# Performance work log

Measured on AMD Instinct MI355X. Metric: run time of the kernel, lower is better.

Reference implementation:

```python
import jax, jax.numpy as jnp
import numpy as np

B, S, H, E, ID, OD, RD = 128, 256, 512, 128, 30000, 64, 32
IN = H + E + 1 + OD  # rnn_input_dim: weighted + embedded + rate + online feats


def setup_inputs() -> dict:
    key = jax.random.key(0)
    ks = jax.random.split(key, 18)
    sc = 0.02
    inp = {}
    inp['input_id'] = jax.random.randint(ks[0], (B, 1), 0, ID, dtype=jnp.int32)
    inp['input_rate'] = jax.random.uniform(ks[1], (B, 1), jnp.float32)
    inp['hidden'] = jax.random.normal(ks[2], (1, B, H), jnp.float32) * 0.1
    inp['encoder_outputs'] = jax.random.normal(ks[3], (S, B, H), jnp.float32) * 0.1
    inp['attn_mask'] = (jax.random.uniform(ks[4], (B, S)) > 0.3).astype(jnp.int32).at[:, 0].set(1)
    inp['constraint_vec'] = (jax.random.uniform(ks[5], (B, ID)) > 0.5).astype(jnp.float32).at[:, 0].set(1.0)
    inp['online_features'] = jax.random.normal(ks[6], (B, OD), jnp.float32) * 0.1
    inp['rid_features'] = jax.random.normal(ks[7], (B, RD), jnp.float32) * 0.1
    inp['emb'] = jax.random.normal(ks[8], (ID, E), jnp.float32) * sc
    inp['attn_W'] = jax.random.normal(ks[9], (2 * H, H), jnp.float32) * sc
    inp['attn_b'] = jnp.zeros((H,), jnp.float32)
    inp['v_W'] = jax.random.normal(ks[10], (H,), jnp.float32) * sc
    inp['W_ih'] = jax.random.normal(ks[11], (3 * H, IN), jnp.float32) * sc
    inp['b_ih'] = jnp.zeros((3 * H,), jnp.float32)
    inp['W_hh'] = jax.random.normal(ks[12], (3 * H, H), jnp.float32) * sc
    inp['b_hh'] = jnp.zeros((3 * H,), jnp.float32)
    inp['fc_id_W'] = jax.random.normal(ks[13], (ID, H), jnp.float32) * sc
    inp['fc_id_b'] = jnp.zeros((ID,), jnp.float32)
    inp['tan_W'] = jax.random.normal(ks[14], (H, E + H), jnp.float32) * sc
    inp['tan_b'] = jnp.zeros((H,), jnp.float32)
    inp['rate_W'] = jax.random.normal(ks[15], (1, H + RD), jnp.float32) * sc
    inp['rate_b'] = jnp.zeros((1,), jnp.float32)
    return inp


def reference(input_id, input_rate, hidden, encoder_outputs, attn_mask, constraint_vec,
              online_features, rid_features, emb, attn_W, attn_b, v_W, W_ih, b_ih,
              W_hh, b_hh, fc_id_W, fc_id_b, tan_W, tan_b, rate_W, rate_b):
    h = hidden[0]                                    # [B,H]
    embedded = emb[input_id[:, 0]]                   # [B,E] (dropout p=0 -> identity)
    # --- attention ---
    enc = jnp.transpose(encoder_outputs, (1, 0, 2))  # [B,S,H]
    hid_rep = jnp.broadcast_to(h[:, None, :], (B, S, H))
    energy = jnp.tanh(jnp.concatenate([hid_rep, enc], axis=2) @ attn_W + attn_b)  # [B,S,H]
    score = energy @ v_W                             # [B,S]
    score = jnp.where(attn_mask == 0, jnp.float32(-1e10), score)
    a = jax.nn.softmax(score, axis=1)                # [B,S]
    weighted = jnp.einsum('bs,bsh->bh', a, enc)      # [B,H]
    # --- GRU step (torch gate order r,z,n) ---
    rnn_in = jnp.concatenate([weighted, embedded, input_rate, online_features], axis=1)  # [B,IN]
    gi = rnn_in @ W_ih.T + b_ih                      # [B,3H]
    gh = h @ W_hh.T + b_hh                           # [B,3H]
    r = jax.nn.sigmoid(gi[:, :H] + gh[:, :H])
    z = jax.nn.sigmoid(gi[:, H:2 * H] + gh[:, H:2 * H])
    n = jnp.tanh(gi[:, 2 * H:] + r * gh[:, 2 * H:])
    h_new = (1.0 - z) * n + z * h                    # [B,H]
    # --- masked log softmax over id_size ---
    logits = h_new @ fc_id_W.T + fc_id_b             # [B,ID]
    maxes = jnp.max(logits, axis=1, keepdims=True)
    x_exp = jnp.exp(logits - maxes) * constraint_vec
    x_sum = jnp.sum(x_exp, axis=1, keepdims=True)
    ratio_safe = jnp.where(constraint_vec > 0, x_exp / x_sum, 1.0)
    prediction_id = jnp.where(constraint_vec > 0, jnp.log(ratio_safe), -jnp.inf)  # [B,ID]
    # --- tandem rate head ---
    max_id = jnp.argmax(prediction_id, axis=1)
    id_emb = emb[max_id]                             # [B,E]
    rate_in = jax.nn.relu(jnp.concatenate([id_emb, h_new], axis=1) @ tan_W.T + tan_b)  # [B,H]
    prediction_rate = jax.nn.sigmoid(jnp.concatenate([rate_in, rid_features], axis=1) @ rate_W.T + rate_b)  # [B,1]
    return prediction_id, prediction_rate, h_new[None]  # hidden: [1,B,H]
```

## Files before the change

### kernel.cpp

```cpp
#include <hip/hip_runtime.h>
#include <math.h>

typedef __attribute__((ext_vector_type(8))) short short8;
typedef __attribute__((ext_vector_type(4))) float f32x4;
typedef __attribute__((ext_vector_type(4))) unsigned int u32x4;

constexpr int kB  = 128;
constexpr int kS  = 256;
constexpr int kH  = 512;
constexpr int kE  = 128;
constexpr int kID = 30000;
constexpr int kOD = 64;
constexpr int kRD = 32;
constexpr int kIN = kH + kE + 1 + kOD;
constexpr int kG  = 3 * kH;
constexpr int kNC = 10;

constexpr int O_PRE  = 0;
constexpr int O_RNN  = O_PRE + kB * kH;
constexpr int O_GI   = O_RNN + kB * kIN;
constexpr int O_GH   = O_GI + kB * kG;
constexpr int O_HNEW = O_GH + kB * kG;
constexpr int O_W2F  = O_HNEW + kB * kH;
constexpr int O_AH   = O_W2F + 32 * 4096;
constexpr int O_AL   = O_AH + 8 * 4096;
constexpr int O_SM   = O_AL + 8 * 4096;
constexpr int O_SS   = O_SM + kB * kNC;
constexpr int O_SBV  = O_SS + kB * kNC;
constexpr int O_SBI  = O_SBV + kB * kNC;
constexpr int O_ENCF = O_SBI + kB * kNC;
constexpr int O_SC8  = O_GI;
constexpr int O_GP   = O_ENCF;
constexpr int O_GPH  = O_GP + 8 * kB * kG;
constexpr int O_RP   = O_PRE;

constexpr float kNegSentinel = -1.0e30f;

__device__ __forceinline__ float fast_tanh(float x) {
    float e = __expf(2.f * x);
    return 1.f - 2.f / (e + 1.f);
}
__device__ __forceinline__ unsigned int f2bf(float x) {
    unsigned int u = __builtin_bit_cast(unsigned int, x);
    return (u + 0x7fffu + ((u >> 16) & 1u)) >> 16;
}
__device__ __forceinline__ float bfval(float x) {
    return __builtin_bit_cast(float, f2bf(x) << 16);
}
__device__ __forceinline__ unsigned int pack2(float a, float b) {
    return f2bf(a) | (f2bf(b) << 16);
}

__global__ __launch_bounds__(256) void k_prep(
    const float* __restrict__ enc, const float* __restrict__ attn_W,
    const float* __restrict__ attn_b, const float* __restrict__ hidden,
    float* __restrict__ ws, unsigned int* __restrict__ wsu) {
    __shared__ unsigned int SMEM[16 * 260];
    const int blk = blockIdx.x;
    const int tid = threadIdx.x;
    if (blk < 256) {
        const int l16 = tid & 15;
        const int cb0 = ((tid >> 4) & 3) * 8 + (tid >> 6) * 32;
        const float* base = enc + ((size_t)(blk * 8) * 16 + l16) * kH + cb0;
        unsigned int* dstb = wsu + O_ENCF + (size_t)(blk * 8) * 4096;
        float4 a[2][8];
        auto ld = [&](int buf, int t) {
            const float* rp = base + (size_t)t * 16 * kH;
#pragma unroll
            for (int p = 0; p < 4; ++p) {
                a[buf][2 * p]     = *(const float4*)(rp + p * 128);
                a[buf][2 * p + 1] = *(const float4*)(rp + p * 128 + 4);
            }
        };
        auto stt = [&](int buf, int t) {
            unsigned int* d = dstb + (size_t)t * 4096;
#pragma unroll
            for (int p = 0; p < 4; ++p) {
                float4 x = a[buf][2 * p], y = a[buf][2 * p + 1];
                u32x4 o = {pack2(x.x, x.y), pack2(x.z, x.w),
                           pack2(y.x, y.y), pack2(y.z, y.w)};
                *(u32x4*)(d + (p * 256 + tid) * 4) = o;
            }
        };
        ld(0, 0);
#pragma unroll
        for (int t = 0; t < 8; ++t) {
            if (t < 7) ld((t + 1) & 1, t + 1);
            stt(t & 1, t);
        }
    } else if (blk < 288) {
        const int rbh = blk - 256;
        const int h0 = rbh * 16;
        const int hh = tid & 15, pg = tid >> 4;
#pragma unroll
        for (int pass = 0; pass < 16; ++pass) {
            int p = pg + pass * 16;
            float a = attn_W[(kH + 2 * p) * kH + h0 + hh];
            float b = attn_W[(kH + 2 * p + 1) * kH + h0 + hh];
            SMEM[hh * 260 + p] = pack2(a, b);
        }
        __syncthreads();
        unsigned int* dst = wsu + O_W2F + (size_t)rbh * 4096;
#pragma unroll
        for (int pass = 0; pass < 4; ++pass) {
            int idx4 = pass * 256 + tid;
            int l16 = idx4 & 15, quad = (idx4 >> 4) & 3, step = idx4 >> 6;
            const unsigned int* p = &SMEM[l16 * 260 + step * 16 + quad * 4];
            u32x4 v = {p[0], p[1], p[2], p[3]};
            *(u32x4*)(dst + idx4 * 4) = v;
        }
    } else {
        float* hl = (float*)SMEM;
        int idx = blk - 288;
        int b = idx >> 1, half = idx & 1;
        int h = half * 256 + tid;
        hl[tid]       = hidden[b * kH + tid];
        hl[tid + 256] = hidden[b * kH + tid + 256];
        __syncthreads();
        float acc0 = attn_b[h], acc1 = 0.f;
        for (int k0 = 0; k0 < kH; k0 += 16) {
            float wv[16];
#pragma unroll
            for (int j = 0; j < 16; ++j) wv[j] = attn_W[(k0 + j) * kH + h];
#pragma unroll
            for (int j = 0; j < 8; ++j) {
                acc0 += hl[k0 + j] * wv[j];
                acc1 += hl[k0 + 8 + j] * wv[8 + j];
            }
        }
        ws[O_PRE + b * kH + h] = acc0 + acc1;
    }
}

__global__ __launch_bounds__(256) void k_attn(
    const unsigned int* __restrict__ encf, const unsigned int* __restrict__ w2f,
    const float* __restrict__ vW, float* __restrict__ ws) {
    __shared__ float red[128 * 33];
    const int i = blockIdx.x;
    const int s    = (i & 7) + 8 * (i >> 6);
    const int hblk = (i >> 3) & 7;
    const int tid = threadIdx.x;
    const int w = tid >> 6, L = tid & 63;
    const int quad = L >> 4, l16 = L & 15;
    const int wm = w >> 1, wn = w & 1;
    const unsigned int* ap[4];
    const unsigned int* bp[2];
#pragma unroll
    for (int mt = 0; mt < 4; ++mt)
        ap[mt] = encf + (size_t)(s * 8 + wm * 4 + mt) * 4096 + L * 4;
#pragma unroll
    for (int nt = 0; nt < 2; ++nt)
        bp[nt] = w2f + (size_t)(hblk * 4 + wn * 2 + nt) * 4096 + L * 4;
    f32x4 acc[4][2] = {};
    u32x4 abuf[2][4], bbuf[2][2];
#pragma unroll
    for (int t = 0; t < 4; ++t) abuf[0][t] = *(const u32x4*)(ap[t]);
#pragma unroll
    for (int t = 0; t < 2; ++t) bbuf[0][t] = *(const u32x4*)(bp[t]);
#pragma unroll
    for (int step = 0; step < 16; ++step) {
        const int cur = step & 1, nxt = cur ^ 1;
        if (step < 15) {
            const int off = (step + 1) * 256;
#pragma unroll
            for (int t = 0; t < 4; ++t) abuf[nxt][t] = *(const u32x4*)(ap[t] + off);
#pragma unroll
            for (int t = 0; t < 2; ++t) bbuf[nxt][t] = *(const u32x4*)(bp[t] + off);
        }
#pragma unroll
        for (int mt = 0; mt < 4; ++mt)
#pragma unroll
            for (int nt = 0; nt < 2; ++nt)
                acc[mt][nt] = __builtin_amdgcn_mfma_f32_16x16x32_bf16(
                    __builtin_bit_cast(short8, abuf[cur][mt]),
                    __builtin_bit_cast(short8, bbuf[cur][nt]), acc[mt][nt], 0, 0, 0);
    }
#pragma unroll
    for (int mt = 0; mt < 4; ++mt)
#pragma unroll
        for (int rg = 0; rg < 4; ++rg) {
            int row = wm * 64 + mt * 16 + quad * 4 + rg;
            const float* prep = &ws[O_PRE + row * kH + hblk * 64 + wn * 32];
            const float* vp = &vW[hblk * 64 + wn * 32];
            float p = 0.f;
#pragma unroll
            for (int nt = 0; nt < 2; ++nt) {
                int hc = nt * 16 + l16;
                p += vp[hc] * fast_tanh(acc[mt][nt][rg] + prep[hc]);
            }
            red[row * 33 + wn * 16 + l16] = p;
        }
    __syncthreads();
    if (tid < 128) {
        float sum = 0.f;
#pragma unroll
        for (int c = 0; c < 32; ++c) sum += red[tid * 33 + c];
        ws[O_SC8 + hblk * (kB * kS) + tid * kS + s] = sum;
    }
}

__global__ __launch_bounds__(256) void k_soft_weight(
    const float* __restrict__ enc, const int* __restrict__ mask,
    const int* __restrict__ input_id, const float* __restrict__ input_rate,
    const float* __restrict__ online, const float* __restrict__ emb,
    float* __restrict__ ws) {
    int b = blockIdx.x, hg = blockIdx.y, tid = threadIdx.x;
    __shared__ float aa[kS];
    __shared__ float sm[256];
    __shared__ float4 red4[16 * 16];
    float v = 0.f;
#pragma unroll
    for (int h8 = 0; h8 < 8; ++h8)
        v += ws[O_SC8 + h8 * (kB * kS) + b * kS + tid];
    if (mask[b * kS + tid] == 0) v = -1e10f;
    sm[tid] = v;
    __syncthreads();
    for (int o = 128; o > 0; o >>= 1) {
        if (tid < o) sm[tid] = fmaxf(sm[tid], sm[tid + o]);
        __syncthreads();
    }
    float M = sm[0];
    __syncthreads();
    float e = __expf(v - M);
    sm[tid] = e;
    __syncthreads();
    for (int o = 128; o > 0; o >>= 1) {
        if (tid < o) sm[tid] += sm[tid + o];
        __syncthreads();
    }
    aa[tid] = e / sm[0];
    __syncthreads();
    int lane = tid & 15, sg = tid >> 4;
    int col4 = hg * 16 + lane;
    const float4* enc4 = (const float4*)enc;
    float4 acc = {0.f, 0.f, 0.f, 0.f};
    for (int s = sg; s < kS; s += 16) {
        float a = aa[s];
        float4 e4 = enc4[(s * kB + b) * (kH / 4) + col4];
        acc.x += a * e4.x; acc.y += a * e4.y; acc.z += a * e4.z; acc.w += a * e4.w;
    }
    red4[sg * 16 + lane] = acc;
    __syncthreads();
    if (sg == 0) {
        float4 o = {0.f, 0.f, 0.f, 0.f};
#pragma unroll
        for (int j = 0; j < 16; ++j) {
            float4 r = red4[j * 16 + lane];
            o.x += r.x; o.y += r.y; o.z += r.z; o.w += r.w;
        }
        float* dst = &ws[O_RNN + b * kIN + col4 * 4];
        dst[0] = o.x; dst[1] = o.y; dst[2] = o.z; dst[3] = o.w;
    }
    if (hg == 0)
        for (int idx = tid; idx < kE + 1 + kOD; idx += 256) {
            int pos = kH + idx;
            float vv;
            if (idx < kE)       vv = emb[input_id[b] * kE + idx];
            else if (idx == kE) vv = input_rate[b];
            else                vv = online[b * kOD + (idx - kE - 1)];
            ws[O_RNN + b * kIN + pos] = vv;
        }
}

__global__ __launch_bounds__(256, 2) void k_gates(
    const float* __restrict__ rnn, const float* __restrict__ W_ih,
    const float* __restrict__ hid, const float* __restrict__ W_hh,
    float* __restrict__ ws) {
    __shared__ float As[16][132];
    __shared__ float Bs[16][132];
    const float* A;  const float* Bm;  float* Cp;
    int K, kChunk;
    if (blockIdx.y == 0) { A = rnn; Bm = W_ih; Cp = ws + O_GP;  K = kIN; kChunk = 96; }
    else                 { A = hid; Bm = W_hh; Cp = ws + O_GPH; K = kH;  kChunk = 64; }
    Cp += (size_t)blockIdx.z * (kB * kG);
    const int n0 = blockIdx.x * 128;
    const int k0 = blockIdx.z * kChunk;
    const int k1 = min(K, k0 + kChunk);
    const int tid = threadIdx.x;
    const int ri = tid >> 4, ci = tid & 15;
    const int sr = tid >> 1, sc = tid & 1;
    const int nrow = n0 + sr;
    float acc[8][8] = {};
    for (int kt = k0; kt < k1; kt += 16) {
        int kbase = kt + sc * 8;
        if (kt + 16 <= k1) {
            const float* ap = &A[sr * K + kbase];
            float4 a0 = *(const float4*)ap;
            float4 a1 = *(const float4*)(ap + 4);
            As[sc * 8 + 0][sr] = a0.x; As[sc * 8 + 1][sr] = a0.y;
            As[sc * 8 + 2][sr] = a0.z; As[sc * 8 + 3][sr] = a0.w;
            As[sc * 8 + 4][sr] = a1.x; As[sc * 8 + 5][sr] = a1.y;
            As[sc * 8 + 6][sr] = a1.z; As[sc * 8 + 7][sr] = a1.w;
            const float* bp = &Bm[(long)nrow * K + kbase];
            float4 b0 = *(const float4*)bp;
            float4 b1 = *(const float4*)(bp + 4);
            Bs[sc * 8 + 0][sr] = b0.x; Bs[sc * 8 + 1][sr] = b0.y;
            Bs[sc * 8 + 2][sr] = b0.z; Bs[sc * 8 + 3][sr] = b0.w;
            Bs[sc * 8 + 4][sr] = b1.x; Bs[sc * 8 + 5][sr] = b1.y;
            Bs[sc * 8 + 6][sr] = b1.z; Bs[sc * 8 + 7][sr] = b1.w;
        } else {
#pragma unroll
            for (int jj = 0; jj < 8; ++jj) {
                int k = kbase + jj;
                As[sc * 8 + jj][sr] = (k < k1) ? A[sr * K + k] : 0.f;
                Bs[sc * 8 + jj][sr] = (k < k1) ? Bm[(long)nrow * K + k] : 0.f;
            }
        }
        __syncthreads();
#pragma unroll
        for (int kk = 0; kk < 16; ++kk) {
            float a[8], b[8];
            *(float4*)&a[0] = *(const float4*)&As[kk][ri * 4];
            *(float4*)&a[4] = *(const float4*)&As[kk][64 + ri * 4];
            *(float4*)&b[0] = *(const float4*)&Bs[kk][ci * 4];
            *(float4*)&b[4] = *(const float4*)&Bs[kk][64 + ci * 4];
#pragma unroll
            for (int rr = 0; rr < 8; ++rr)
#pragma unroll
                for (int cc = 0; cc < 8; ++cc) acc[rr][cc] += a[rr] * b[cc];
        }
        __syncthreads();
    }
#pragma unroll
    for (int rh = 0; rh < 2; ++rh)
#pragma unroll
        for (int ii = 0; ii < 4; ++ii) {
            int m = rh * 64 + ri * 4 + ii;
#pragma unroll
            for (int ch = 0; ch < 2; ++ch) {
                float4 v = {acc[rh * 4 + ii][ch * 4 + 0], acc[rh * 4 + ii][ch * 4 + 1],
                            acc[rh * 4 + ii][ch * 4 + 2], acc[rh * 4 + ii][ch * 4 + 3]};
                *(float4*)&Cp[(size_t)m * kG + n0 + ch * 64 + ci * 4] = v;
            }
        }
}

__global__ __launch_bounds__(128) void k_gru(const float* __restrict__ hidden,
                                             const float* __restrict__ b_ih,
                                             const float* __restrict__ b_hh,
                                             float* __restrict__ ws,
                                             unsigned int* __restrict__ wsu,
                                             float* __restrict__ outh) {
    int idx = blockIdx.x * 128 + threadIdx.x;
    int b = idx >> 8, pair = idx & 255;
    int j0 = pair * 2;
    const float* gpi = &ws[O_GP  + (size_t)b * kG + j0];
    const float* gph = &ws[O_GPH + (size_t)b * kG + j0];
    float2 gir = {0.f, 0.f}, giz = {0.f, 0.f}, gin = {0.f, 0.f};
    float2 ghr = {0.f, 0.f}, ghz = {0.f, 0.f}, ghn = {0.f, 0.f};
#pragma unroll
    for (int z = 0; z < 8; ++z) {
        size_t off = (size_t)z * (kB * kG);
        float2 a0 = *(const float2*)(gpi + off);
        float2 a1 = *(const float2*)(gpi + off + kH);
        float2 a2 = *(const float2*)(gpi + off + 2 * kH);
        float2 c0 = *(const float2*)(gph + off);
        float2 c1 = *(const float2*)(gph + off + kH);
        float2 c2 = *(const float2*)(gph + off + 2 * kH);
        gir.x += a0.x; gir.y += a0.y; giz.x += a1.x; giz.y += a1.y;
        gin.x += a2.x; gin.y += a2.y;
        ghr.x += c0.x; ghr.y += c0.y; ghz.x += c1.x; ghz.y += c1.y;
        ghn.x += c2.x; ghn.y += c2.y;
    }
    float hn2[2];
#pragma unroll
    for (int t = 0; t < 2; ++t) {
        int j = j0 + t;
        float gi_r = t ? gir.y : gir.x;
        float gi_z = t ? giz.y : giz.x;
        float gi_n = t ? gin.y : gin.x;
        float gh_r = t ? ghr.y : ghr.x;
        float gh_z = t ? ghz.y : ghz.x;
        float gh_n = t ? ghn.y : ghn.x;
        float gr = gi_r + b_ih[j] + gh_r + b_hh[j];
        float gz = gi_z + b_ih[kH + j] + gh_z + b_hh[kH + j];
        float r = 1.f / (1.f + expf(-gr));
        float z = 1.f / (1.f + expf(-gz));
        float n = tanhf(gi_n + b_ih[2 * kH + j] + r * (gh_n + b_hh[2 * kH + j]));
        float hn = (1.f - z) * n + z * hidden[b * kH + j];
        ws[O_HNEW + b * kH + j] = hn;
        outh[b * kH + j] = hn;
        hn2[t] = hn;
    }
    int fidx = (b >> 4) * 4096 +
               ((pair >> 4) * 4 + ((pair >> 2) & 3)) * 64 + (b & 15) * 4 + (pair & 3);
    wsu[O_AH + fidx] = pack2(hn2[0], hn2[1]);
    wsu[O_AL + fidx] = pack2(hn2[0] - bfval(hn2[0]), hn2[1] - bfval(hn2[1]));
}

__global__ __launch_bounds__(256) void k_logits(
    const unsigned int* __restrict__ wsu, const float* __restrict__ Wm,
    const float* __restrict__ bias, float* __restrict__ C) {
    __shared__ unsigned int BH[4][64 * 20];
    __shared__ unsigned int BL[4][64 * 20];
    const unsigned int* Ahp = wsu + O_AH;
    const unsigned int* Alp = wsu + O_AL;
    const int n0 = blockIdx.x * 64;
    const int tid = threadIdx.x;
    const int w = tid >> 6, L = tid & 63;
    const int quad = L >> 4, l16 = L & 15;
    const int r = tid >> 2, seg = tid & 3;
    const int nrow = n0 + r;
    auto stage = [&](int buf, int step) {
        float bv[8] = {};
        if (nrow < kID) {
            const float* bp = &Wm[(long)nrow * kH + step * 32 + seg * 8];
            *(float4*)&bv[0] = *(const float4*)(bp);
            *(float4*)&bv[4] = *(const float4*)(bp + 4);
        }
        u32x4 oh = {pack2(bv[0], bv[1]), pack2(bv[2], bv[3]),
                    pack2(bv[4], bv[5]), pack2(bv[6], bv[7])};
        u32x4 ol = {pack2(bv[0] - bfval(bv[0]), bv[1] - bfval(bv[1])),
                    pack2(bv[2] - bfval(bv[2]), bv[3] - bfval(bv[3])),
                    pack2(bv[4] - bfval(bv[4]), bv[5] - bfval(bv[5])),
                    pack2(bv[6] - bfval(bv[6]), bv[7] - bfval(bv[7]))};
        *(u32x4*)&BH[buf][r * 20 + seg * 4] = oh;
        *(u32x4*)&BL[buf][r * 20 + seg * 4] = ol;
    };
    stage(0, 0);
    stage(1, 1);
    stage(2, 2);
    __syncthreads();
    f32x4 acc[2][4] = {};
    for (int step = 0; step < 16; ++step) {
        const int cur = step & 3;
        short8 ah[2], al[2], bh[4], bl[4];
#pragma unroll
        for (int mt = 0; mt < 2; ++mt) {
            int off = (w * 2 + mt) * 4096 + step * 256 + L * 4;
            ah[mt] = __builtin_bit_cast(short8, *(const u32x4*)(Ahp + off));
            al[mt] = __builtin_bit_cast(short8, *(const u32x4*)(Alp + off));
        }
        const unsigned int* ch = BH[cur];
        const unsigned int* cl = BL[cur];
#pragma unroll
        for (int nt = 0; nt < 4; ++nt) {
            bh[nt] = __builtin_bit_cast(short8,
                *(const u32x4*)(ch + (nt * 16 + l16) * 20 + quad * 4));
            bl[nt] = __builtin_bit_cast(short8,
                *(const u32x4*)(cl + (nt * 16 + l16) * 20 + quad * 4));
        }
#pragma unroll
        for (int mt = 0; mt < 2; ++mt)
#pragma unroll
            for (int nt = 0; nt < 4; ++nt) {
                acc[mt][nt] = __builtin_amdgcn_mfma_f32_16x16x32_bf16(
                    al[mt], bh[nt], acc[mt][nt], 0, 0, 0);
                acc[mt][nt] = __builtin_amdgcn_mfma_f32_16x16x32_bf16(
                    ah[mt], bl[nt], acc[mt][nt], 0, 0, 0);
                acc[mt][nt] = __builtin_amdgcn_mfma_f32_16x16x32_bf16(
                    ah[mt], bh[nt], acc[mt][nt], 0, 0, 0);
            }
        if (step + 3 < 16) stage((step + 3) & 3, step + 3);
        __syncthreads();
    }
#pragma unroll
    for (int mt = 0; mt < 2; ++mt)
#pragma unroll
        for (int rg = 0; rg < 4; ++rg) {
            int m = w * 32 + mt * 16 + quad * 4 + rg;
#pragma unroll
            for (int nt = 0; nt < 4; ++nt) {
                int n = n0 + nt * 16 + l16;
                if (n < kID) C[(long)m * kID + n] = acc[mt][nt][rg] + bias[n];
            }
        }
}

__global__ __launch_bounds__(256) void k_stats1(const float* __restrict__ logits,
                                                const float* __restrict__ cvec,
                                                float* __restrict__ ws) {
    int c = blockIdx.x, b = blockIdx.y, tid = threadIdx.x;
    constexpr int chunkE = kID / kNC;
    constexpr int chunk4 = chunkE / 4;
    const float4* lp = (const float4*)(logits + (long)b * kID + c * chunkE);
    const float4* cp = (const float4*)(cvec + (long)b * kID + c * chunkE);
    __shared__ float smm[256], sms[256], smb[256];
    __shared__ int smi[256];
    float m = -INFINITY, s = 0.f, bv = -INFINITY;
    int bi = kID;
    for (int i = tid; i < chunk4; i += 256) {
        float4 l4 = lp[i];
        float4 c4 = cp[i];
        float le[4] = {l4.x, l4.y, l4.z, l4.w};
        float ce[4] = {c4.x, c4.y, c4.z, c4.w};
#pragma unroll
        for (int jj = 0; jj < 4; ++jj) {
            float l = le[jj];
            if (l > m) { s *= __expf(m - l); m = l; }
            if (ce[jj] > 0.f) {
                s += __expf(l - m);
                if (l > bv) { bv = l; bi = c * chunkE + i * 4 + jj; }
            }
        }
    }
    smm[tid] = m; sms[tid] = s; smb[tid] = bv; smi[tid] = bi;
    __syncthreads();
    for (int o = 128; o > 0; o >>= 1) {
        if (tid < o) {
            float m1 = smm[tid], s1 = sms[tid];
            float m2 = smm[tid + o], s2 = sms[tid + o];
            float M = fmaxf(m1, m2);
            sms[tid] = s1 * __expf(m1 - M) + s2 * __expf(m2 - M);
            smm[tid] = M;
            float ov = smb[tid + o]; int oi = smi[tid + o];
            if (ov > smb[tid] || (ov == smb[tid] && oi < smi[tid])) {
                smb[tid] = ov; smi[tid] = oi;
            }
        }
        __syncthreads();
    }
    if (tid == 0) {
        ws[O_SM + b * kNC + c]  = smm[0];
        ws[O_SS + b * kNC + c]  = sms[0];
        ws[O_SBV + b * kNC + c] = smb[0];
        ((int*)ws)[O_SBI + b * kNC + c] = smi[0];
    }
}

__global__ __launch_bounds__(256) void k_finalize(const float* __restrict__ cvec,
                                                  const float* __restrict__ ws,
                                                  float* __restrict__ out) {
    int b = blockIdx.y;
    int i4 = blockIdx.x * 256 + threadIdx.x;
    if (i4 >= kID / 4) return;
    float M = -INFINITY;
#pragma unroll
    for (int c = 0; c < kNC; ++c) M = fmaxf(M, ws[O_SM + b * kNC + c]);
    float S = 0.f;
#pragma unroll
    for (int c = 0; c < kNC; ++c)
        S += ws[O_SS + b * kNC + c] * __expf(ws[O_SM + b * kNC + c] - M);
    float off = M + logf(S);
    float4* op = (float4*)(out + (long)b * kID);
    const float4* cp = (const float4*)(cvec + (long)b * kID);
    float4 l = op[i4];
    float4 c = cp[i4];
    l.x = (c.x > 0.f) ? l.x - off : kNegSentinel;
    l.y = (c.y > 0.f) ? l.y - off : kNegSentinel;
    l.z = (c.z > 0.f) ? l.z - off : kNegSentinel;
    l.w = (c.w > 0.f) ? l.w - off : kNegSentinel;
    op[i4] = l;
}

__global__ __launch_bounds__(256) void k_rate1(
    const float* __restrict__ emb, const float* __restrict__ tanW,
    const float* __restrict__ tanb, const float* __restrict__ rateW,
    float* __restrict__ ws) {
    constexpr int KK = kE + kH;
    int b = blockIdx.x, g = blockIdx.y, tid = threadIdx.x;
    __shared__ float xin[KK];
    __shared__ float red[8];
    float bv = -INFINITY;
    int mid = kID;
#pragma unroll
    for (int c = 0; c < kNC; ++c) {
        float ov = ws[O_SBV + b * kNC + c];
        int oi = ((const int*)ws)[O_SBI + b * kNC + c];
        if (ov > bv || (ov == bv && oi < mid)) { bv = ov; mid = oi; }
    }
    for (int idx = tid; idx < KK; idx += 256)
        xin[idx] = (idx < kE) ? emb[(size_t)mid * kE + idx]
                              : ws[O_HNEW + b * kH + (idx - kE)];
    __syncthreads();
    int grp = tid >> 5, lane = tid & 31;
    int jbase = g * 64 + grp * 8;
    const float* wr = &tanW[(size_t)jbase * KK + lane];
    float acc[8] = {};
#pragma unroll
    for (int t = 0; t < KK / 32; ++t) {
        float xv = xin[lane + 32 * t];
#pragma unroll
        for (int r = 0; r < 8; ++r) acc[r] += xv * wr[r * KK + 32 * t];
    }
    float gsum = 0.f;
#pragma unroll
    for (int r = 0; r < 8; ++r) {
        float a = acc[r];
#pragma unroll
        for (int o = 16; o > 0; o >>= 1) a += __shfl_down(a, o, 32);
        if (lane == 0) gsum += fmaxf(a + tanb[jbase + r], 0.f) * rateW[jbase + r];
    }
    if (lane == 0) red[grp] = gsum;
    __syncthreads();
    if (tid == 0) {
        float s = 0.f;
#pragma unroll
        for (int r = 0; r < 8; ++r) s += red[r];
        ws[O_RP + b * 8 + g] = s;
    }
}

__global__ __launch_bounds__(128) void k_rate2(
    const float* __restrict__ rid, const float* __restrict__ rateW,
    const float* __restrict__ rateb, const float* __restrict__ ws,
    float* __restrict__ out) {
    int b = threadIdx.x;
    float acc = rateb[0];
#pragma unroll
    for (int g = 0; g < 8; ++g) acc += ws[O_RP + b * 8 + g];
#pragma unroll
    for (int k = 0; k < kRD; ++k) acc += rid[b * kRD + k] * rateW[kH + k];
    out[b] = 1.f / (1.f + expf(-acc));
}

extern "C" void kernel_launch(void* const* d_in, const int* in_sizes, int n_in,
                              void* d_out, int out_size, void* d_ws, size_t ws_size,
                              hipStream_t stream) {
    const int*   input_id   = (const int*)  d_in[0];
    const float* input_rate = (const float*)d_in[1];
    const float* hidden     = (const float*)d_in[2];
    const float* enc        = (const float*)d_in[3];
    const int*   attn_mask  = (const int*)  d_in[4];
    const float* cvec       = (const float*)d_in[5];
    const float* online     = (const float*)d_in[6];
    const float* rid        = (const float*)d_in[7];
    const float* emb        = (const float*)d_in[8];
    const float* attn_W     = (const float*)d_in[9];
    const float* attn_b     = (const float*)d_in[10];
    const float* vW         = (const float*)d_in[11];
    const float* W_ih       = (const float*)d_in[12];
    const float* b_ih       = (const float*)d_in[13];
    const float* W_hh       = (const float*)d_in[14];
    const float* b_hh       = (const float*)d_in[15];
    const float* fc_id_W    = (const float*)d_in[16];
    const float* fc_id_b    = (const float*)d_in[17];
    const float* tan_W      = (const float*)d_in[18];
    const float* tan_b      = (const float*)d_in[19];
    const float* rate_W     = (const float*)d_in[20];
    const float* rate_b     = (const float*)d_in[21];

    float* ws         = (float*)d_ws;
    unsigned int* wsu = (unsigned int*)d_ws;
    float* out        = (float*)d_out;
    float* out_pid    = out;
    float* out_rate   = out + kB * kID;
    float* out_h      = out + kB * kID + kB;

    k_prep<<<544, 256, 0, stream>>>(enc, attn_W, attn_b, hidden, ws, wsu);
    k_attn<<<2048, 256, 0, stream>>>(wsu + O_ENCF, wsu + O_W2F, vW, ws);
    k_soft_weight<<<dim3(128, 8), 256, 0, stream>>>(enc, attn_mask, input_id,
                                                    input_rate, online, emb, ws);
    k_gates<<<dim3(kG / 128, 2, 8), 256, 0, stream>>>(ws + O_RNN, W_ih, hidden, W_hh, ws);
    k_gru<<<256, 128, 0, stream>>>(hidden, b_ih, b_hh, ws, wsu, out_h);
    k_logits<<<dim3((kID + 63) / 64), 256, 0, stream>>>(wsu, fc_id_W, fc_id_b, out_pid);
    k_stats1<<<dim3(kNC, 128), 256, 0, stream>>>(out_pid, cvec, ws);
    k_finalize<<<dim3(30, 128), 256, 0, stream>>>(cvec, ws, out_pid);
    k_rate1<<<dim3(128, 8), 256, 0, stream>>>(emb, tan_W, tan_b, rate_W, ws);
    k_rate2<<<1, 128, 0, stream>>>(rid, rate_W, rate_b, ws, out_rate);
}
```

Baseline: 352.5 us.

## Restructure logits GEMM to stream fc weights through registers with swapped operands

The logits kernel now lets each wave own 32 vocabulary rows and all 128 batch rows. fc_id_W is loaded straight from global memory into registers with a two-stage register double buffer, and the split-bf16 conversion happens in registers. This removes the LDS staging buffers and the per-step __syncthreads. Weights become the MFMA A operand and hidden the B operand, so each lane's accumulator holds four consecutive vocab ids, which enables float4 bias loads and float4 output stores. The cost is higher register pressure from 16 accumulators, and every wave re-reads the full packed hidden matrix from global/L2 at each step.

Result: no change. 353.6 us (+0.3%).

```diff
diff --git a/kernel.cpp b/kernel.cpp
--- a/kernel.cpp
+++ b/kernel.cpp
@@ -391,80 +391,87 @@
 __global__ __launch_bounds__(256) void k_logits(
     const unsigned int* __restrict__ wsu, const float* __restrict__ Wm,
     const float* __restrict__ bias, float* __restrict__ C) {
-    __shared__ unsigned int BH[4][64 * 20];
-    __shared__ unsigned int BL[4][64 * 20];
     const unsigned int* Ahp = wsu + O_AH;
     const unsigned int* Alp = wsu + O_AL;
-    const int n0 = blockIdx.x * 64;
     const int tid = threadIdx.x;
     const int w = tid >> 6, L = tid & 63;
     const int quad = L >> 4, l16 = L & 15;
-    const int r = tid >> 2, seg = tid & 3;
-    const int nrow = n0 + r;
-    auto stage = [&](int buf, int step) {
-        float bv[8] = {};
-        if (nrow < kID) {
-            const float* bp = &Wm[(long)nrow * kH + step * 32 + seg * 8];
-            *(float4*)&bv[0] = *(const float4*)(bp);
-            *(float4*)&bv[4] = *(const float4*)(bp + 4);
-        }
-        u32x4 oh = {pack2(bv[0], bv[1]), pack2(bv[2], bv[3]),
-                    pack2(bv[4], bv[5]), pack2(bv[6], bv[7])};
-        u32x4 ol = {pack2(bv[0] - bfval(bv[0]), bv[1] - bfval(bv[1])),
-                    pack2(bv[2] - bfval(bv[2]), bv[3] - bfval(bv[3])),
-                    pack2(bv[4] - bfval(bv[4]), bv[5] - bfval(bv[5])),
-                    pack2(bv[6] - bfval(bv[6]), bv[7] - bfval(bv[7]))};
-        *(u32x4*)&BH[buf][r * 20 + seg * 4] = oh;
-        *(u32x4*)&BL[buf][r * 20 + seg * 4] = ol;
+    const int wavebase = blockIdx.x * 128 + w * 32;
+    const float* wp[2];
+    bool wvalid[2];
+#pragma unroll
+    for (int mt = 0; mt < 2; ++mt) {
+        int row = wavebase + mt * 16 + l16;
+        wvalid[mt] = row < kID;
+        wp[mt] = Wm + (size_t)(wvalid[mt] ? row : 0) * kH + quad * 8;
+    }
+    f32x4 acc[2][8] = {};
+    float4 wbuf[2][2][2];
+    auto ldW = [&](int buf, int step) {
+#pragma unroll
+        for (int mt = 0; mt < 2; ++mt) {
+            float4 x = {0.f, 0.f, 0.f, 0.f}, y = {0.f, 0.f, 0.f, 0.f};
+            if (wvalid[mt]) {
+                x = *(const float4*)(wp[mt] + step * 32);
+                y = *(const float4*)(wp[mt] + step * 32 + 4);
+            }
+            wbuf[buf][mt][0] = x;
+            wbuf[buf][mt][1] = y;
+        }
     };
-    stage(0, 0);
-    stage(1, 1);
-    stage(2, 2);
-    __syncthreads();
-    f32x4 acc[2][4] = {};
+    ldW(0, 0);
+#pragma unroll
     for (int step = 0; step < 16; ++step) {
-        const int cur = step & 3;
-        short8 ah[2], al[2], bh[4], bl[4];
+        const int cur = step & 1;
+        if (step < 15) ldW(cur ^ 1, step + 1);
+        short8 wh[2], wl[2];
 #pragma unroll
         for (int mt = 0; mt < 2; ++mt) {
-            int off = (w * 2 + mt) * 4096 + step * 256 + L * 4;
-            ah[mt] = __builtin_bit_cast(short8, *(const u32x4*)(Ahp + off));
-            al[mt] = __builtin_bit_cast(short8, *(const u32x4*)(Alp + off));
-        }
-        const unsigned int* ch = BH[cur];
-        const unsigned int* cl = BL[cur];
-#pragma unroll
-        for (int nt = 0; nt < 4; ++nt) {
-            bh[nt] = __builtin_bit_cast(short8,
-                *(const u32x4*)(ch + (nt * 16 + l16) * 20 + quad * 4));
-            bl[nt] = __builtin_bit_cast(short8,
-                *(const u32x4*)(cl + (nt * 16 + l16) * 20 + quad * 4));
+            float x0 = wbuf[cur][mt][0].x, x1 = wbuf[cur][mt][0].y;
+            float x2 = wbuf[cur][mt][0].z, x3 = wbuf[cur][mt][0].w;
+            float x4 = wbuf[cur][mt][1].x, x5 = wbuf[cur][mt][1].y;
+            float x6 = wbuf[cur][mt][1].z, x7 = wbuf[cur][mt][1].w;
+            u32x4 hi = {pack2(x0, x1), pack2(x2, x3), pack2(x4, x5), pack2(x6, x7)};
+            u32x4 lo = {pack2(x0 - bfval(x0), x1 - bfval(x1)),
+                        pack2(x2 - bfval(x2), x3 - bfval(x3)),
+                        pack2(x4 - bfval(x4), x5 - bfval(x5)),
+                        pack2(x6 - bfval(x6), x7 - bfval(x7))};
+            wh[mt] = __builtin_bit_cast(short8, hi);
+            wl[mt] = __builtin_bit_cast(short8, lo);
+        }
+        short8 hh[8], hl[8];
+#pragma unroll
+        for (int bt = 0; bt < 8; ++bt) {
+            int off = bt * 4096 + step * 256 + L * 4;
+            hh[bt] = __builtin_bit_cast(short8, *(const u32x4*)(Ahp + off));
+            hl[bt] = __builtin_bit_cast(short8, *(const u32x4*)(Alp + off));
         }
 #pragma unroll
         for (int mt = 0; mt < 2; ++mt)
 #pragma unroll
-            for (int nt = 0; nt < 4; ++nt) {
-                acc[mt][nt] = __builtin_amdgcn_mfma_f32_16x16x32_bf16(
-                    al[mt], bh[nt], acc[mt][nt], 0, 0, 0);
-                acc[mt][nt] = __builtin_amdgcn_mfma_f32_16x16x32_bf16(
-                    ah[mt], bl[nt], acc[mt][nt], 0, 0, 0);
-                acc[mt][nt] = __builtin_amdgcn_mfma_f32_16x16x32_bf16(
-                    ah[mt], bh[nt], acc[mt][nt], 0, 0, 0);
-            }
-        if (step + 3 < 16) stage((step + 3) & 3, step + 3);
-        __syncthreads();
-    }
-#pragma unroll
-    for (int mt = 0; mt < 2; ++mt)
-#pragma unroll
-        for (int rg = 0; rg < 4; ++rg) {
-            int m = w * 32 + mt * 16 + quad * 4 + rg;
-#pragma unroll
-            for (int nt = 0; nt < 4; ++nt) {
-                int n = n0 + nt * 16 + l16;
-                if (n < kID) C[(long)m * kID + n] = acc[mt][nt][rg] + bias[n];
-            }
-        }
+            for (int bt = 0; bt < 8; ++bt) {
+                acc[mt][bt] = __builtin_amdgcn_mfma_f32_16x16x32_bf16(
+                    wl[mt], hh[bt], acc[mt][bt], 0, 0, 0);
+                acc[mt][bt] = __builtin_amdgcn_mfma_f32_16x16x32_bf16(
+                    wh[mt], hl[bt], acc[mt][bt], 0, 0, 0);
+                acc[mt][bt] = __builtin_amdgcn_mfma_f32_16x16x32_bf16(
+                    wh[mt], hh[bt], acc[mt][bt], 0, 0, 0);
+            }
+    }
+#pragma unroll
+    for (int mt = 0; mt < 2; ++mt) {
+        int id4 = wavebase + mt * 16 + quad * 4;
+        if (id4 < kID) {
+            float4 b4 = *(const float4*)(bias + id4);
+#pragma unroll
+            for (int bt = 0; bt < 8; ++bt) {
+                int b = bt * 16 + l16;
+                f32x4 v = acc[mt][bt];
+                float4 o = {v[0] + b4.x, v[1] + b4.y, v[2] + b4.z, v[3] + b4.w};
+                *(float4*)(C + (size_t)b * kID + id4) = o;
+            }
+        }
+    }
 }
 
 __global__ __launch_bounds__(256) void k_stats1(const float* __restrict__ logits,
@@ -643,7 +650,7 @@
                                                     input_rate, online, emb, ws);
     k_gates<<<dim3(kG / 128, 2, 8), 256, 0, stream>>>(ws + O_RNN, W_ih, hidden, W_hh, ws);
     k_gru<<<256, 128, 0, stream>>>(hidden, b_ih, b_hh, ws, wsu, out_h);
-    k_logits<<<dim3((kID + 63) / 64), 256, 0, stream>>>(wsu, fc_id_W, fc_id_b, out_pid);
+    k_logits<<<dim3((kID + 127) / 128), 256, 0, stream>>>(wsu, fc_id_W, fc_id_b, out_pid);
     k_stats1<<<dim3(kNC, 128), 256, 0, stream>>>(out_pid, cvec, ws);
     k_finalize<<<dim3(30, 128), 256, 0, stream>>>(cvec, ws, out_pid);
     k_rate1<<<dim3(128, 8), 256, 0, stream>>>(emb, tan_W, tan_b, rate_W, ws);
```
